# Performance work log

Measured on AMD Instinct MI355X. Metric: run time of the kernel, lower is better.

## Reference

```python
import jax, jax.numpy as jnp
import numpy as np

N = 100000   # nodes
E = 1600000  # edges
IN, H, C = 128, 128, 40


def setup_inputs() -> dict:
    key = jax.random.key(0)
    ks = jax.random.split(key, 8)
    feat = jax.random.normal(ks[0], (N, IN), jnp.float32)
    src = jax.random.randint(ks[1], (E,), 0, N, jnp.int32)
    dst = jax.random.randint(ks[2], (E,), 0, N, jnp.int32)
    # Glorot-ish init like dgl GraphConv.reset_parameters
    W0 = jax.random.normal(ks[3], (IN, H), jnp.float32) * (1.0 / np.sqrt(IN))
    W1 = jax.random.normal(ks[4], (H, H), jnp.float32) * (1.0 / np.sqrt(H))
    W2 = jax.random.normal(ks[5], (H, C), jnp.float32) * (1.0 / np.sqrt(H))
    b0 = jnp.zeros((H,), jnp.float32)
    b1 = jnp.zeros((H,), jnp.float32)
    b2 = jnp.zeros((C,), jnp.float32)
    return {"feat": feat, "src": src, "dst": dst,
            "W0": W0, "b0": b0, "W1": W1, "b1": b1, "W2": W2, "b2": b2}


def _graph_conv(h, src, dst, W, b):
    # dgl GraphConv with norm='both': D_out^{-1/2} pre-scale, sum-aggregate,
    # D_in^{-1/2} post-scale; degrees clamped to min 1. Weight applied before
    # aggregation (in_feats >= out_feats path) -- math is identical either way.
    ones = jnp.ones((src.shape[0],), h.dtype)
    deg_out = jnp.maximum(jax.ops.segment_sum(ones, src, num_segments=N), 1.0)
    deg_in = jnp.maximum(jax.ops.segment_sum(ones, dst, num_segments=N), 1.0)
    h = h * (deg_out ** -0.5)[:, None]
    h = h @ W                                   # [N, out]
    agg = jax.ops.segment_sum(h[src], dst, num_segments=N)  # gather+scatter
    return agg * (deg_in ** -0.5)[:, None] + b


def reference(feat, src, dst, W0, b0, W1, b1, W2, b2):
    h = jax.nn.relu(_graph_conv(feat, src, dst, W0, b0))  # dropout p=0 -> identity
    h = jax.nn.relu(_graph_conv(h, src, dst, W1, b1))
    return _graph_conv(h, src, dst, W2, b2)
```

## Files before the change

kernel.cpp:

```cpp
#include <hip/hip_runtime.h>

#define NN 100000
#define EE 1600000
#define ELLW 64
#define NXCD 8
#define RNG ((NN + NXCD - 1) / NXCD)
#define GEMMN ((NN + 31) / 32)
#define BUILDN ((EE / 256) * NXCD)
#define H40P 48

__device__ __forceinline__ unsigned int pack_bf2(float a, float b) {
    unsigned int ua = __float_as_uint(a);
    ua += 0x7FFFu + ((ua >> 16) & 1u);
    unsigned int ub = __float_as_uint(b);
    ub += 0x7FFFu + ((ub >> 16) & 1u);
    return (ua >> 16) | (ub & 0xFFFF0000u);
}

__device__ __forceinline__ void nt_store_f2(float* p, float x, float y) {
    unsigned long long v = (unsigned long long)__float_as_uint(x) |
                           ((unsigned long long)__float_as_uint(y) << 32);
    __builtin_nontemporal_store(v, (unsigned long long*)p);
}

__device__ __forceinline__ void gemm128_body(const float* __restrict__ X, const int* __restrict__ dout,
                                             const float* __restrict__ W, unsigned int* __restrict__ Y,
                                             int n, int row0, int tid, float* Xs, int scaled) {
    const float4* X4 = (const float4*)X;
#pragma unroll
    for (int idx = tid; idx < 1024; idx += 256) {
        int r = idx & 31, c4 = idx >> 5;
        int row = row0 + r;
        float4 v = make_float4(0.f, 0.f, 0.f, 0.f);
        float s = 0.f;
        if (row < n) {
            v = X4[(size_t)row * 32 + c4];
            s = scaled ? rsqrtf((float)max(1, dout[row])) : 1.f;
        }
        Xs[(c4 * 4 + 0) * 32 + r] = v.x * s;
        Xs[(c4 * 4 + 1) * 32 + r] = v.y * s;
        Xs[(c4 * 4 + 2) * 32 + r] = v.z * s;
        Xs[(c4 * 4 + 3) * 32 + r] = v.w * s;
    }
    __syncthreads();
    int cg = tid & 31;
    int rg = tid >> 5;
    float a[4][4];
#pragma unroll
    for (int r = 0; r < 4; ++r)
#pragma unroll
        for (int c = 0; c < 4; ++c) a[r][c] = 0.f;
    const float4* W4 = (const float4*)W;
#pragma unroll 4
    for (int k = 0; k < 128; ++k) {
        float4 xv = *(const float4*)&Xs[k * 32 + rg * 4];
        float4 wv = W4[k * 32 + cg];
        float xr[4] = {xv.x, xv.y, xv.z, xv.w};
        float wc[4] = {wv.x, wv.y, wv.z, wv.w};
#pragma unroll
        for (int r = 0; r < 4; ++r)
#pragma unroll
            for (int c = 0; c < 4; ++c) a[r][c] = fmaf(xr[r], wc[c], a[r][c]);
    }
    int rbase = row0 + rg * 4;
    uint2* Y2 = (uint2*)Y;
#pragma unroll
    for (int r = 0; r < 4; ++r) {
        if (rbase + r < n) {
            Y2[(size_t)(rbase + r) * 32 + cg] =
                make_uint2(pack_bf2(a[r][0], a[r][1]), pack_bf2(a[r][2], a[r][3]));
        }
    }
}

__global__ __launch_bounds__(256) void k_build_gemm0(const int* __restrict__ src, const int* __restrict__ dst,
                                                     int* __restrict__ din, int* __restrict__ dout,
                                                     int* __restrict__ ell,
                                                     const float* __restrict__ X, const float* __restrict__ W,
                                                     unsigned int* __restrict__ Y) {
    __shared__ float Xs[128 * 32];
    int tid = threadIdx.x;
    if (blockIdx.x < GEMMN) {
        gemm128_body(X, nullptr, W, Y, NN, blockIdx.x * 32, tid, Xs, 0);
        return;
    }
    int idx = blockIdx.x - GEMMN;
    int r = idx & (NXCD - 1);
    int slice = idx >> 3;
    int i = slice * 256 + tid;
    if (i >= EE) return;
    int s = __builtin_nontemporal_load(&src[i]);
    int d = __builtin_nontemporal_load(&dst[i]);
    int lo = r * RNG, hi = lo + RNG;
    if (d >= lo && d < hi) {
        int p = atomicAdd(&din[d], 1);
        if (p < ELLW) ell[(size_t)d * ELLW + p] = s;
    }
    if (s >= lo && s < hi) {
        atomicAdd(&dout[s], 1);
    }
}

__global__ __launch_bounds__(256) void k_gemm128(const float* __restrict__ X, const int* __restrict__ dout,
                                                 const float* __restrict__ W, unsigned int* __restrict__ Y, int n) {
    __shared__ float Xs[128 * 32];
    gemm128_body(X, dout, W, Y, n, blockIdx.x * 32, threadIdx.x, Xs, 1);
}

__global__ __launch_bounds__(320) void k_gemm40(const float* __restrict__ X, const int* __restrict__ dout,
                                                const float* __restrict__ W, float* __restrict__ Y, int n) {
    __shared__ float Xs[128 * 64];
    int tid = threadIdx.x;
    int row0 = blockIdx.x * 64;
    const float4* X4 = (const float4*)X;
    for (int idx = tid; idx < 2048; idx += 320) {
        int r = idx & 63, c4 = idx >> 6;
        int row = row0 + r;
        float4 v = make_float4(0.f, 0.f, 0.f, 0.f);
        float s = 0.f;
        if (row < n) { v = X4[(size_t)row * 32 + c4]; s = rsqrtf((float)max(1, dout[row])); }
        Xs[(c4 * 4 + 0) * 64 + r] = v.x * s;
        Xs[(c4 * 4 + 1) * 64 + r] = v.y * s;
        Xs[(c4 * 4 + 2) * 64 + r] = v.z * s;
        Xs[(c4 * 4 + 3) * 64 + r] = v.w * s;
    }
    __syncthreads();
    int cg = tid % 20;
    int rg = tid / 20;
    float a0x=0,a0y=0, a1x=0,a1y=0, a2x=0,a2y=0, a3x=0,a3y=0;
    const float2* W2 = (const float2*)W;
#pragma unroll 4
    for (int k = 0; k < 128; ++k) {
        float4 xv = *(const float4*)&Xs[k * 64 + rg * 4];
        float2 wv = W2[k * 20 + cg];
        a0x += xv.x * wv.x; a0y += xv.x * wv.y;
        a1x += xv.y * wv.x; a1y += xv.y * wv.y;
        a2x += xv.z * wv.x; a2y += xv.z * wv.y;
        a3x += xv.w * wv.x; a3y += xv.w * wv.y;
    }
    int rbase = row0 + rg * 4;
    float2* Y2 = (float2*)Y;
    if (rbase + 0 < n) Y2[(size_t)(rbase + 0) * 24 + cg] = make_float2(a0x, a0y);
    if (rbase + 1 < n) Y2[(size_t)(rbase + 1) * 24 + cg] = make_float2(a1x, a1y);
    if (rbase + 2 < n) Y2[(size_t)(rbase + 2) * 24 + cg] = make_float2(a2x, a2y);
    if (rbase + 3 < n) Y2[(size_t)(rbase + 3) * 24 + cg] = make_float2(a3x, a3y);
}

__global__ __launch_bounds__(256) void k_gather128(const unsigned int* __restrict__ h, const int* __restrict__ din,
                                                   const int* __restrict__ dout, const int* __restrict__ ell,
                                                   const float* __restrict__ b, float* __restrict__ out,
                                                   int n, int do_relu, int so_mode) {
    int wv = threadIdx.x >> 6, lane = threadIdx.x & 63;
    int v = blockIdx.x * 4 + wv;
    if (v >= n) return;
    int dv = din[v];
    int cnt = min(dv, ELLW);
    int cl = ell[(size_t)v * ELLW + lane];
    int cls = (lane < cnt) ? cl : 0;
    float scl = 1.f;
    if (so_mode) scl = rsqrtf((float)max(1, dout[cls]));
    float sx = 0.f, sy = 0.f;
    for (int j = 0; j < cnt; j += 8) {
        int cc[8]; float mk[8]; unsigned int t[8];
#pragma unroll
        for (int k = 0; k < 8; ++k) {
            int jj = j + k;
            int jc = jj < cnt ? jj : cnt - 1;
            cc[k] = __shfl(cls, jc);
            float sw = __shfl(scl, jc);
            mk[k] = (jj < cnt) ? sw : 0.f;
        }
#pragma unroll
        for (int k = 0; k < 8; ++k)
            t[k] = h[(size_t)cc[k] * 64 + lane];
#pragma unroll
        for (int k = 0; k < 8; ++k) {
            float x = __uint_as_float(t[k] << 16);
            float y = __uint_as_float(t[k] & 0xFFFF0000u);
            sx = fmaf(mk[k], x, sx);
            sy = fmaf(mk[k], y, sy);
        }
    }
    float sc = rsqrtf((float)max(1, dv));
    float2 bb = ((const float2*)b)[lane];
    float ox = sx * sc + bb.x;
    float oy = sy * sc + bb.y;
    if (do_relu) { ox = fmaxf(ox, 0.f); oy = fmaxf(oy, 0.f); }
    nt_store_f2((float*)((float2*)out + (size_t)v * 64 + lane), ox, oy);
}

__global__ __launch_bounds__(256) void k_gather40(const float* __restrict__ h, const int* __restrict__ din,
                                                  const int* __restrict__ ell,
                                                  const float* __restrict__ b, float* __restrict__ out, int n) {
    int wv = threadIdx.x >> 6, lane = threadIdx.x & 63;
    int v = blockIdx.x * 4 + wv;
    if (v >= n) return;
    int dv = din[v];
    int cnt = min(dv, ELLW);
    int cl = ell[(size_t)v * ELLW + lane];
    int cls = (lane < cnt) ? cl : 0;
    float s = 0.f;
    for (int j = 0; j < cnt; j += 8) {
        int cc[8]; float mk[8]; float t[8];
#pragma unroll
        for (int k = 0; k < 8; ++k) {
            int jj = j + k;
            cc[k] = __shfl(cls, jj < cnt ? jj : cnt - 1);
            mk[k] = (jj < cnt) ? 1.f : 0.f;
        }
        if (lane < 40) {
#pragma unroll
            for (int k = 0; k < 8; ++k) t[k] = h[(size_t)cc[k] * H40P + lane];
#pragma unroll
            for (int k = 0; k < 8; ++k) s = fmaf(mk[k], t[k], s);
        }
    }
    if (lane < 40) {
        out[(size_t)v * 40 + lane] = s * rsqrtf((float)max(1, dv)) + b[lane];
    }
}

extern "C" void kernel_launch(void* const* d_in, const int* in_sizes, int n_in,
                              void* d_out, int out_size, void* d_ws, size_t ws_size,
                              hipStream_t stream) {
    const float* feat = (const float*)d_in[0];
    const int*   src  = (const int*)d_in[1];
    const int*   dst  = (const int*)d_in[2];
    const float* W0   = (const float*)d_in[3];
    const float* b0   = (const float*)d_in[4];
    const float* W1   = (const float*)d_in[5];
    const float* b1   = (const float*)d_in[6];
    const float* W2   = (const float*)d_in[7];
    const float* b2   = (const float*)d_in[8];
    float* out = (float*)d_out;

    char* w = (char*)d_ws;
    int*   din       = (int*)w;    w += (size_t)NN * 4;
    int*   dout      = (int*)w;    w += (size_t)NN * 4;
    int*   ell       = (int*)w;    w += (size_t)NN * ELLW * 4;
    unsigned int* h2 = (unsigned int*)w; w += (size_t)NN * 128 * 2;
    float* h40       = (float*)w;  w += (size_t)NN * H40P * 4;
    float* agg       = (float*)w;  w += (size_t)NN * 128 * 4;

    hipMemsetAsync(d_ws, 0, (size_t)NN * 8, stream);

    int gath_grid = (NN + 3) / 4;

    k_build_gemm0<<<GEMMN + BUILDN, 256, 0, stream>>>(src, dst, din, dout, ell, feat, W0, h2);
    k_gather128<<<gath_grid, 256, 0, stream>>>(h2, din, dout, ell, b0, agg, NN, 1, 1);
    k_gemm128<<<GEMMN, 256, 0, stream>>>(agg, dout, W1, h2, NN);
    k_gather128<<<gath_grid, 256, 0, stream>>>(h2, din, dout, ell, b1, agg, NN, 1, 0);
    k_gemm40<<<(NN + 63) / 64, 320, 0, stream>>>(agg, dout, W2, h40, NN);
    k_gather40<<<gath_grid, 256, 0, stream>>>(h40, din, ell, b2, out, NN);
}
```

Baseline: 569.0 us.

## Store layer-3 features as bf16 and interleave GEMM blocks with graph build

The 40-wide output projection is now written as packed bf16 in 128-byte rows instead of fp32 rows padded to 48. The final gather reads these bf16 values and widens them to fp32 before accumulating, roughly halving the bytes fetched per neighbour and keeping each row within one cache line. Separately, the fused build+GEMM0 launch now places one GEMM block after every 16 edge-build blocks instead of running all GEMM blocks first, so compute-heavy and atomic-heavy work run side by side. The cost is bf16 rounding of the last layer's pre-aggregation features, which adds error to the final output.

```diff
diff --git a/kernel.cpp b/kernel.cpp
--- a/kernel.cpp
+++ b/kernel.cpp
@@ -7,7 +7,6 @@
 #define RNG ((NN + NXCD - 1) / NXCD)
 #define GEMMN ((NN + 31) / 32)
 #define BUILDN ((EE / 256) * NXCD)
-#define H40P 48
 
 __device__ __forceinline__ unsigned int pack_bf2(float a, float b) {
     unsigned int ua = __float_as_uint(a);
@@ -80,11 +79,12 @@
                                                      unsigned int* __restrict__ Y) {
     __shared__ float Xs[128 * 32];
     int tid = threadIdx.x;
-    if (blockIdx.x < GEMMN) {
-        gemm128_body(X, nullptr, W, Y, NN, blockIdx.x * 32, tid, Xs, 0);
+    int q = blockIdx.x / 17, rem = blockIdx.x % 17;
+    if (rem == 16) {
+        gemm128_body(X, nullptr, W, Y, NN, q * 32, tid, Xs, 0);
         return;
     }
-    int idx = blockIdx.x - GEMMN;
+    int idx = q * 16 + rem;
     int r = idx & (NXCD - 1);
     int slice = idx >> 3;
     int i = slice * 256 + tid;
@@ -108,7 +108,7 @@
 }
 
 __global__ __launch_bounds__(320) void k_gemm40(const float* __restrict__ X, const int* __restrict__ dout,
-                                                const float* __restrict__ W, float* __restrict__ Y, int n) {
+                                                const float* __restrict__ W, unsigned int* __restrict__ Y, int n) {
     __shared__ float Xs[128 * 64];
     int tid = threadIdx.x;
     int row0 = blockIdx.x * 64;
@@ -139,11 +139,10 @@
         a3x += xv.w * wv.x; a3y += xv.w * wv.y;
     }
     int rbase = row0 + rg * 4;
-    float2* Y2 = (float2*)Y;
-    if (rbase + 0 < n) Y2[(size_t)(rbase + 0) * 24 + cg] = make_float2(a0x, a0y);
-    if (rbase + 1 < n) Y2[(size_t)(rbase + 1) * 24 + cg] = make_float2(a1x, a1y);
-    if (rbase + 2 < n) Y2[(size_t)(rbase + 2) * 24 + cg] = make_float2(a2x, a2y);
-    if (rbase + 3 < n) Y2[(size_t)(rbase + 3) * 24 + cg] = make_float2(a3x, a3y);
+    if (rbase + 0 < n) Y[(size_t)(rbase + 0) * 32 + cg] = pack_bf2(a0x, a0y);
+    if (rbase + 1 < n) Y[(size_t)(rbase + 1) * 32 + cg] = pack_bf2(a1x, a1y);
+    if (rbase + 2 < n) Y[(size_t)(rbase + 2) * 32 + cg] = pack_bf2(a2x, a2y);
+    if (rbase + 3 < n) Y[(size_t)(rbase + 3) * 32 + cg] = pack_bf2(a3x, a3y);
 }
 
 __global__ __launch_bounds__(256) void k_gather128(const unsigned int* __restrict__ h, const int* __restrict__ din,
@@ -189,7 +188,7 @@
     nt_store_f2((float*)((float2*)out + (size_t)v * 64 + lane), ox, oy);
 }
 
-__global__ __launch_bounds__(256) void k_gather40(const float* __restrict__ h, const int* __restrict__ din,
+__global__ __launch_bounds__(256) void k_gather40(const unsigned short* __restrict__ h, const int* __restrict__ din,
                                                   const int* __restrict__ ell,
                                                   const float* __restrict__ b, float* __restrict__ out, int n) {
     int wv = threadIdx.x >> 6, lane = threadIdx.x & 63;
@@ -201,7 +200,7 @@
     int cls = (lane < cnt) ? cl : 0;
     float s = 0.f;
     for (int j = 0; j < cnt; j += 8) {
-        int cc[8]; float mk[8]; float t[8];
+        int cc[8]; float mk[8]; unsigned short t[8];
 #pragma unroll
         for (int k = 0; k < 8; ++k) {
             int jj = j + k;
@@ -210,9 +209,10 @@
         }
         if (lane < 40) {
 #pragma unroll
-            for (int k = 0; k < 8; ++k) t[k] = h[(size_t)cc[k] * H40P + lane];
-#pragma unroll
-            for (int k = 0; k < 8; ++k) s = fmaf(mk[k], t[k], s);
+            for (int k = 0; k < 8; ++k) t[k] = h[(size_t)cc[k] * 64 + lane];
+#pragma unroll
+            for (int k = 0; k < 8; ++k)
+                s = fmaf(mk[k], __uint_as_float((unsigned int)t[k] << 16), s);
         }
     }
     if (lane < 40) {
@@ -239,17 +239,17 @@
     int*   dout      = (int*)w;    w += (size_t)NN * 4;
     int*   ell       = (int*)w;    w += (size_t)NN * ELLW * 4;
     unsigned int* h2 = (unsigned int*)w; w += (size_t)NN * 128 * 2;
-    float* h40       = (float*)w;  w += (size_t)NN * H40P * 4;
+    unsigned int* h40 = (unsigned int*)w; w += (size_t)NN * 32 * 4;
     float* agg       = (float*)w;  w += (size_t)NN * 128 * 4;
 
     hipMemsetAsync(d_ws, 0, (size_t)NN * 8, stream);
 
     int gath_grid = (NN + 3) / 4;
 
-    k_build_gemm0<<<GEMMN + BUILDN, 256, 0, stream>>>(src, dst, din, dout, ell, feat, W0, h2);
+    k_build_gemm0<<<GEMMN * 17, 256, 0, stream>>>(src, dst, din, dout, ell, feat, W0, h2);
     k_gather128<<<gath_grid, 256, 0, stream>>>(h2, din, dout, ell, b0, agg, NN, 1, 1);
     k_gemm128<<<GEMMN, 256, 0, stream>>>(agg, dout, W1, h2, NN);
     k_gather128<<<gath_grid, 256, 0, stream>>>(h2, din, dout, ell, b1, agg, NN, 1, 0);
     k_gemm40<<<(NN + 63) / 64, 320, 0, stream>>>(agg, dout, W2, h40, NN);
-    k_gather40<<<gath_grid, 256, 0, stream>>>(h40, din, ell, b2, out, NN);
-}
+    k_gather40<<<gath_grid, 256, 0, stream>>>((const unsigned short*)h40, din, ell, b2, out, NN);
+}
```

Result: no change. 567.0 us (-0.3%).
